# Kernel tuning notes

Hardware: AMD Instinct MI355X
Metric: run time of the kernel (lower is better)

The kernel has to match this reference:

```python
import jax, jax.numpy as jnp
import numpy as np

N = 100000   # nodes
E = 1600000  # edges (avg degree 16)
D = 128      # in_dim == out_dim (residual path)
NEG_SLOPE = 0.1


def setup_inputs() -> dict:
    key = jax.random.key(0)
    k1, k2, k3 = jax.random.split(key, 3)
    x = jax.random.normal(k1, (N, D), dtype=jnp.float32)
    edge_index = jax.random.randint(k2, (2, E), 0, N, dtype=jnp.int32)
    # GCNConv linear weight (stored as [in, out]; PyG uses x @ W^T with [out, in] — same math)
    W = jax.random.normal(k3, (D, D), dtype=jnp.float32) / np.sqrt(D).astype(np.float32)
    b = jnp.zeros((D,), dtype=jnp.float32)
    return {"x": x, "edge_index": edge_index, "W": W, "b": b}


def reference(x, edge_index, W, b):
    n = x.shape[0]
    # add self loops (GCNConv add_self_loops=True)
    loops = jnp.arange(n, dtype=edge_index.dtype)
    src = jnp.concatenate([edge_index[0], loops])
    dst = jnp.concatenate([edge_index[1], loops])
    # symmetric normalization: deg computed on destination index (PyG gcn_norm)
    deg = jax.ops.segment_sum(jnp.ones_like(dst, dtype=x.dtype), dst, num_segments=n)
    dinv = jnp.where(deg > 0, jax.lax.rsqrt(deg), 0.0)
    norm = dinv[src] * dinv[dst]                     # [E+N]
    # transform-then-propagate: small GEMM, then gather/scale/scatter
    h = x @ W                                        # [N, D]
    msgs = h[src] * norm[:, None]                    # [E+N, D] gather + scale
    agg = jax.ops.segment_sum(msgs, dst, num_segments=n) + b  # scatter-add
    act = jnp.where(agg >= 0, agg, NEG_SLOPE * agg)  # leaky_relu(0.1)
    return act + x                                   # residual (in_dim == out_dim)
```

## Files before the change

### kernel.cpp

```cpp
#include <hip/hip_runtime.h>
#include <hip/hip_bf16.h>

#define D 128
#define NEG_SLOPE 0.1f
#define BSHIFT 7
#define BSIZE 128
#define HALF 64
#define SRCBITS 17
#define SRCMASK 0x1FFFF
#define NBMAX 784
#define REGION 2432
#define SRCCAP 1536

typedef __attribute__((ext_vector_type(8))) short bf16x8;
typedef __attribute__((ext_vector_type(4))) float f32x4;
typedef __attribute__((ext_vector_type(2))) float f32x2;

__device__ inline unsigned short f2bf(float f) {
    unsigned u = __builtin_bit_cast(unsigned, f);
    u += 0x7fff + ((u >> 16) & 1);
    return (unsigned short)(u >> 16);
}

__global__ __launch_bounds__(512) void k_scatter2(const int* __restrict__ src, const int* __restrict__ dst,
                                                  int* __restrict__ cursor, int* __restrict__ ebuf,
                                                  int E, int NB,
                                                  const float* __restrict__ W,
                                                  unsigned short* __restrict__ Wt) {
    int b = blockIdx.x;
    int nbE = gridDim.x - 32;
    if (b >= nbE) {
        int tt = (b - nbE) * 512 + threadIdx.x;
        int k = tt >> 7, nn = tt & 127;
        Wt[nn * D + k] = f2bf(W[k * D + nn]);
        return;
    }
    __shared__ int cntL[NBMAX], baseL[NBMAX], curL[NBMAX];
    int t = threadIdx.x;
    for (int i = t; i < NB; i += 512) { cntL[i] = 0; curL[i] = 0; }
    __syncthreads();

    const int4* src4 = (const int4*)src;
    const int4* dst4 = (const int4*)dst;
    int sv[16], dv[16];
    int nval[4];
#pragma unroll
    for (int j = 0; j < 4; j++) {
        int i4 = b * 2048 + j * 512 + t;
        int e = i4 * 4;
        if (e + 4 <= E) {
            int4 s = src4[i4];
            int4 d = dst4[i4];
            sv[j * 4] = s.x; sv[j * 4 + 1] = s.y; sv[j * 4 + 2] = s.z; sv[j * 4 + 3] = s.w;
            dv[j * 4] = d.x; dv[j * 4 + 1] = d.y; dv[j * 4 + 2] = d.z; dv[j * 4 + 3] = d.w;
            nval[j] = 4;
        } else {
            int c = 0;
            for (int k = e; k < E; k++, c++) { sv[j * 4 + c] = src[k]; dv[j * 4 + c] = dst[k]; }
            nval[j] = c;
        }
    }
#pragma unroll
    for (int j = 0; j < 4; j++)
        for (int k = 0; k < nval[j]; k++) atomicAdd(&cntL[dv[j * 4 + k] >> BSHIFT], 1);
    __syncthreads();
    for (int i = t; i < NB; i += 512) {
        int c = cntL[i];
        if (c) baseL[i] = atomicAdd(&cursor[i], c);
    }
    __syncthreads();
#pragma unroll
    for (int j = 0; j < 4; j++)
        for (int k = 0; k < nval[j]; k++) {
            int d = dv[j * 4 + k];
            int bk = d >> BSHIFT;
            int slot = baseL[bk] + atomicAdd(&curL[bk], 1);
            if (slot < REGION)
                ebuf[bk * REGION + slot] = ((d & (BSIZE - 1)) << SRCBITS) | sv[j * 4 + k];
        }
}

__global__ __launch_bounds__(256) void k_gemm(const float* __restrict__ x,
                                              const unsigned short* __restrict__ Wt,
                                              const int* __restrict__ bucketCnt,
                                              const int* __restrict__ ebuf,
                                              unsigned char* __restrict__ h, int n) {
    __shared__ unsigned short Wl[D * 136];
    __shared__ int cntL[BSIZE];
    int t = threadIdx.x;
    if (t < BSIZE) cntL[t] = 0;
    const uint4* Wg4 = (const uint4*)Wt;
#pragma unroll
    for (int j = 0; j < 8; j++) {
        int c = t + 256 * j;
        int row = c >> 4, kg = c & 15;
        *(uint4*)&Wl[row * 136 + kg * 8] = Wg4[row * 16 + kg];
    }
    __syncthreads();

    int estart = blockIdx.x * REGION;
    int ecnt = bucketCnt[blockIdx.x];
    if (ecnt > REGION) ecnt = REGION;
    for (int e = t; e < ecnt; e += 256) atomicAdd(&cntL[ebuf[estart + e] >> SRCBITS], 1);

    int lane = t & 63, wave = t >> 6;
    int quad = lane >> 4, mrow = lane & 15;
    int rbase = blockIdx.x * 128 + wave * 32;

    const float4* x4 = (const float4*)x;
    float4 a0[2][4], a1[2][4];
#pragma unroll
    for (int rt = 0; rt < 2; rt++) {
        int row = rbase + rt * 16 + mrow;
        long rowl = (row < n) ? row : (n - 1);
#pragma unroll
        for (int ks = 0; ks < 4; ks++) {
            long base = rowl * 32 + ks * 8 + quad * 2;
            a0[rt][ks] = x4[base];
            a1[rt][ks] = x4[base + 1];
        }
    }
    bf16x8 af[2][4];
#pragma unroll
    for (int rt = 0; rt < 2; rt++)
#pragma unroll
        for (int ks = 0; ks < 4; ks++) {
            bf16x8 f;
            f[0] = (short)f2bf(a0[rt][ks].x); f[1] = (short)f2bf(a0[rt][ks].y);
            f[2] = (short)f2bf(a0[rt][ks].z); f[3] = (short)f2bf(a0[rt][ks].w);
            f[4] = (short)f2bf(a1[rt][ks].x); f[5] = (short)f2bf(a1[rt][ks].y);
            f[6] = (short)f2bf(a1[rt][ks].z); f[7] = (short)f2bf(a1[rt][ks].w);
            af[rt][ks] = f;
        }

    f32x4 acc[2][8];
#pragma unroll
    for (int rt = 0; rt < 2; rt++)
#pragma unroll
        for (int ct = 0; ct < 8; ct++) acc[rt][ct] = (f32x4){0.f, 0.f, 0.f, 0.f};

#pragma unroll
    for (int ks = 0; ks < 4; ks++) {
#pragma unroll
        for (int ct = 0; ct < 8; ct++) {
            bf16x8 bf = *(bf16x8*)&Wl[(ct * 16 + mrow) * 136 + ks * 32 + quad * 8];
#pragma unroll
            for (int rt = 0; rt < 2; rt++)
                acc[rt][ct] = __builtin_amdgcn_mfma_f32_16x16x32_bf16(af[rt][ks], bf, acc[rt][ct], 0, 0, 0);
        }
    }

    __syncthreads();

#pragma unroll
    for (int rt = 0; rt < 2; rt++) {
#pragma unroll
        for (int reg = 0; reg < 4; reg++) {
            int row = rbase + rt * 16 + quad * 4 + reg;
            if (row < n) {
                int rloc = wave * 32 + rt * 16 + quad * 4 + reg;
                float dv = rsqrtf((float)cntL[rloc] + 1.0f);
                float a[8];
#pragma unroll
                for (int ct = 0; ct < 8; ct++) a[ct] = acc[rt][ct][reg] * dv;
                int w0 = __builtin_amdgcn_cvt_pk_fp8_f32(a[0], a[1], 0, false);
                w0 = __builtin_amdgcn_cvt_pk_fp8_f32(a[2], a[3], w0, true);
                int w1 = __builtin_amdgcn_cvt_pk_fp8_f32(a[4], a[5], 0, false);
                w1 = __builtin_amdgcn_cvt_pk_fp8_f32(a[6], a[7], w1, true);
                uint2 wv; wv.x = (unsigned)w0; wv.y = (unsigned)w1;
                *(uint2*)&h[(long)row * 128 + mrow * 8] = wv;
            }
        }
    }
}

#define ACCV(v)                                                       \
    {                                                                 \
        acc2[0] += __builtin_amdgcn_cvt_pk_f32_fp8((int)(v).x, false);\
        acc2[1] += __builtin_amdgcn_cvt_pk_f32_fp8((int)(v).x, true); \
        acc2[2] += __builtin_amdgcn_cvt_pk_f32_fp8((int)(v).y, false);\
        acc2[3] += __builtin_amdgcn_cvt_pk_f32_fp8((int)(v).y, true); \
        acc2[4] += __builtin_amdgcn_cvt_pk_f32_fp8((int)(v).z, false);\
        acc2[5] += __builtin_amdgcn_cvt_pk_f32_fp8((int)(v).z, true); \
        acc2[6] += __builtin_amdgcn_cvt_pk_f32_fp8((int)(v).w, false);\
        acc2[7] += __builtin_amdgcn_cvt_pk_f32_fp8((int)(v).w, true); \
    }

__global__ __launch_bounds__(256) void k_aggregate(const uint4* __restrict__ h4, const float* __restrict__ x,
                                                   const float* __restrict__ bias,
                                                   const int* __restrict__ bucketCnt, const int* __restrict__ ebuf,
                                                   float* __restrict__ out, int N) {
    __shared__ int srcL[SRCCAP];
    __shared__ int degL[HALF];
    __shared__ int startL[HALF];
    __shared__ int curL[HALF];

    int b = blockIdx.x >> 1, half = blockIdx.x & 1;
    int t = threadIdx.x;
    int nstart = (b << BSHIFT) + half * HALF;
    int estart = b * REGION;
    int ecnt = bucketCnt[b];
    if (ecnt > REGION) ecnt = REGION;

    if (t < HALF) degL[t] = 0;
    __syncthreads();

    int ev[10];
    int ne = 0;
    for (int e = t; e < ecnt; e += 256) ev[ne++] = ebuf[estart + e];
    for (int k = 0; k < ne; k++) {
        int dl = ev[k] >> SRCBITS;
        if ((dl >> 6) == half) atomicAdd(&degL[dl & (HALF - 1)], 1);
    }
    __syncthreads();

    if (t < 64) {
        int d = degL[t];
        int inc = d;
        for (int sh = 1; sh < 64; sh <<= 1) {
            int y = __shfl_up(inc, sh, 64);
            if (t >= sh) inc += y;
        }
        startL[t] = inc - d;
        curL[t] = inc - d;
    }
    __syncthreads();
    for (int k = 0; k < ne; k++) {
        int dl = ev[k] >> SRCBITS;
        if ((dl >> 6) == half) {
            int pos = atomicAdd(&curL[dl & (HALF - 1)], 1);
            if (pos < SRCCAP) srcL[pos] = ev[k] & SRCMASK;
        }
    }
    __syncthreads();

    int wave = t >> 6, lane = t & 63;
    int slot = lane >> 3, chunk = lane & 7;
    for (int nloc = wave; nloc < HALF; nloc += 4) {
        int i = nstart + nloc;
        if (i >= N) break;
        int start = startL[nloc], m = degL[nloc];
        if (start + m > SRCCAP) m = (SRCCAP > start) ? SRCCAP - start : 0;

        f32x2 acc2[8];
#pragma unroll
        for (int r = 0; r < 8; r++) acc2[r] = (f32x2){0.f, 0.f};
        if (slot == 0) {
            uint4 v = h4[(long)i * 8 + chunk];
            ACCV(v);
        }

        int j0 = 0;
        if (m >= 16) {
            int ja = start + slot;
            int e0 = srcL[ja], e1 = srcL[ja + 8];
            for (;;) {
                uint4 v0 = h4[(long)e0 * 8 + chunk];
                uint4 v1 = h4[(long)e1 * 8 + chunk];
                j0 += 16;
                bool more = (j0 + 16 <= m);
                if (more) {
                    int jb = start + j0 + slot;
                    e0 = srcL[jb];
                    e1 = srcL[jb + 8];
                }
                ACCV(v0);
                ACCV(v1);
                if (!more) break;
            }
        }
        if (j0 + 8 <= m) {
            int e = srcL[start + j0 + slot];
            uint4 v = h4[(long)e * 8 + chunk];
            ACCV(v);
            j0 += 8;
        }
        for (int j = j0 + slot; j < m; j += 8) {
            int e = srcL[start + j];
            uint4 v = h4[(long)e * 8 + chunk];
            ACCV(v);
        }

#pragma unroll
        for (int r = 0; r < 8; r++) {
            acc2[r].x += __shfl_xor(acc2[r].x, 8, 64);
            acc2[r].x += __shfl_xor(acc2[r].x, 16, 64);
            acc2[r].x += __shfl_xor(acc2[r].x, 32, 64);
            acc2[r].y += __shfl_xor(acc2[r].y, 8, 64);
            acc2[r].y += __shfl_xor(acc2[r].y, 16, 64);
            acc2[r].y += __shfl_xor(acc2[r].y, 32, 64);
        }

        int s1 = slot >> 1;
        f32x2 eL = (s1 == 0) ? acc2[0] : (s1 == 1) ? acc2[1] : (s1 == 2) ? acc2[2] : acc2[3];
        f32x2 eH = (s1 == 0) ? acc2[4] : (s1 == 1) ? acc2[5] : (s1 == 2) ? acc2[6] : acc2[7];
        float ax = (slot & 1) ? eL.y : eL.x;
        float ay = (slot & 1) ? eH.y : eH.x;

        float di = rsqrtf((float)m + 1.0f);
        int dbase = slot * 16 + chunk * 2;
        float2 bb = *(const float2*)&bias[dbase];
        float2 xv = *(const float2*)&x[(long)i * D + dbase];
        ax = ax * di + bb.x;
        ay = ay * di + bb.y;
        ax = (ax >= 0.f) ? ax : NEG_SLOPE * ax;
        ay = (ay >= 0.f) ? ay : NEG_SLOPE * ay;
        float2 o;
        o.x = ax + xv.x;
        o.y = ay + xv.y;
        *(float2*)&out[(long)i * D + dbase] = o;
    }
}

extern "C" void kernel_launch(void* const* d_in, const int* in_sizes, int n_in,
                              void* d_out, int out_size, void* d_ws, size_t ws_size,
                              hipStream_t stream) {
    const float* x = (const float*)d_in[0];
    const int* edge_index = (const int*)d_in[1];
    const float* W = (const float*)d_in[2];
    const float* bias = (const float*)d_in[3];
    float* out = (float*)d_out;

    int N = in_sizes[0] / D;
    int E = in_sizes[1] / 2;
    const int* src = edge_index;
    const int* dst = edge_index + E;
    int NB = (N + BSIZE - 1) >> BSHIFT;

    char* ws = (char*)d_ws;
    size_t off = 0;
    auto alloc = [&](size_t bytes) {
        void* p = ws + off;
        off += (bytes + 15) & ~(size_t)15;
        return p;
    };
    int* cursor = (int*)alloc((size_t)NB * 4);
    int* ebuf = (int*)alloc((size_t)NB * REGION * 4);
    unsigned short* Wt = (unsigned short*)alloc((size_t)D * D * 2);
    unsigned char* h = (unsigned char*)alloc((size_t)N * D);

    int nbE = (E + 8191) / 8192;

    hipMemsetAsync(cursor, 0, (size_t)NB * 4, stream);
    k_scatter2<<<nbE + 32, 512, 0, stream>>>(src, dst, cursor, ebuf, E, NB, W, Wt);
    k_gemm<<<(N + 127) / 128, 256, 0, stream>>>(x, Wt, cursor, ebuf, h, N);
    k_aggregate<<<NB * 2, 256, 0, stream>>>((const uint4*)h, x, bias, cursor, ebuf, out, N);
}
```

Measured before the change: 209.6 us.

## Use one 512-thread aggregate block per bucket and halve scatter edges per block

The aggregate kernel now processes a whole 128-node bucket per 512-thread block instead of two 64-node halves in 256-thread blocks. This removes the duplicated read and filtering of each bucket's edge list and drops the SRCCAP truncation. The scatter kernel now handles 4096 edges per block with fixed unrolled loops and sentinel-padded tails instead of variable-length inner loops, which doubles its block count. The change trades fewer aggregate blocks and more shared memory per block for less redundant edge work.

```diff
diff --git a/kernel.cpp b/kernel.cpp
--- a/kernel.cpp
+++ b/kernel.cpp
@@ -5,12 +5,10 @@
 #define NEG_SLOPE 0.1f
 #define BSHIFT 7
 #define BSIZE 128
-#define HALF 64
 #define SRCBITS 17
 #define SRCMASK 0x1FFFF
 #define NBMAX 784
 #define REGION 2432
-#define SRCCAP 1536
 
 typedef __attribute__((ext_vector_type(8))) short bf16x8;
 typedef __attribute__((ext_vector_type(4))) float f32x4;
@@ -42,27 +40,27 @@
 
     const int4* src4 = (const int4*)src;
     const int4* dst4 = (const int4*)dst;
-    int sv[16], dv[16];
-    int nval[4];
-#pragma unroll
-    for (int j = 0; j < 4; j++) {
-        int i4 = b * 2048 + j * 512 + t;
+    int sv[8], dv[8];
+#pragma unroll
+    for (int j = 0; j < 2; j++) {
+        int i4 = b * 1024 + j * 512 + t;
         int e = i4 * 4;
+        int4 s, d;
         if (e + 4 <= E) {
-            int4 s = src4[i4];
-            int4 d = dst4[i4];
-            sv[j * 4] = s.x; sv[j * 4 + 1] = s.y; sv[j * 4 + 2] = s.z; sv[j * 4 + 3] = s.w;
-            dv[j * 4] = d.x; dv[j * 4 + 1] = d.y; dv[j * 4 + 2] = d.z; dv[j * 4 + 3] = d.w;
-            nval[j] = 4;
+            s = src4[i4];
+            d = dst4[i4];
         } else {
-            int c = 0;
-            for (int k = e; k < E; k++, c++) { sv[j * 4 + c] = src[k]; dv[j * 4 + c] = dst[k]; }
-            nval[j] = c;
-        }
-    }
-#pragma unroll
-    for (int j = 0; j < 4; j++)
-        for (int k = 0; k < nval[j]; k++) atomicAdd(&cntL[dv[j * 4 + k] >> BSHIFT], 1);
+            s.x = (e < E) ? src[e] : 0;     d.x = (e < E) ? dst[e] : -1;
+            s.y = (e + 1 < E) ? src[e + 1] : 0; d.y = (e + 1 < E) ? dst[e + 1] : -1;
+            s.z = (e + 2 < E) ? src[e + 2] : 0; d.z = (e + 2 < E) ? dst[e + 2] : -1;
+            s.w = (e + 3 < E) ? src[e + 3] : 0; d.w = (e + 3 < E) ? dst[e + 3] : -1;
+        }
+        sv[j * 4 + 0] = s.x; sv[j * 4 + 1] = s.y; sv[j * 4 + 2] = s.z; sv[j * 4 + 3] = s.w;
+        dv[j * 4 + 0] = d.x; dv[j * 4 + 1] = d.y; dv[j * 4 + 2] = d.z; dv[j * 4 + 3] = d.w;
+    }
+#pragma unroll
+    for (int k = 0; k < 8; k++)
+        if (dv[k] >= 0) atomicAdd(&cntL[dv[k] >> BSHIFT], 1);
     __syncthreads();
     for (int i = t; i < NB; i += 512) {
         int c = cntL[i];
@@ -70,14 +68,15 @@
     }
     __syncthreads();
 #pragma unroll
-    for (int j = 0; j < 4; j++)
-        for (int k = 0; k < nval[j]; k++) {
-            int d = dv[j * 4 + k];
+    for (int k = 0; k < 8; k++) {
+        int d = dv[k];
+        if (d >= 0) {
             int bk = d >> BSHIFT;
             int slot = baseL[bk] + atomicAdd(&curL[bk], 1);
             if (slot < REGION)
-                ebuf[bk * REGION + slot] = ((d & (BSIZE - 1)) << SRCBITS) | sv[j * 4 + k];
-        }
+                ebuf[bk * REGION + slot] = ((d & (BSIZE - 1)) << SRCBITS) | sv[k];
+        }
+    }
 }
 
 __global__ __launch_bounds__(256) void k_gemm(const float* __restrict__ x,
@@ -186,61 +185,66 @@
         acc2[7] += __builtin_amdgcn_cvt_pk_f32_fp8((int)(v).w, true); \
     }
 
-__global__ __launch_bounds__(256) void k_aggregate(const uint4* __restrict__ h4, const float* __restrict__ x,
+__global__ __launch_bounds__(512) void k_aggregate(const uint4* __restrict__ h4, const float* __restrict__ x,
                                                    const float* __restrict__ bias,
                                                    const int* __restrict__ bucketCnt, const int* __restrict__ ebuf,
                                                    float* __restrict__ out, int N) {
-    __shared__ int srcL[SRCCAP];
-    __shared__ int degL[HALF];
-    __shared__ int startL[HALF];
-    __shared__ int curL[HALF];
-
-    int b = blockIdx.x >> 1, half = blockIdx.x & 1;
+    __shared__ int srcL[REGION];
+    __shared__ int degL[BSIZE];
+    __shared__ int startL[BSIZE];
+    __shared__ int curL[BSIZE];
+
+    int b = blockIdx.x;
     int t = threadIdx.x;
-    int nstart = (b << BSHIFT) + half * HALF;
+    int nstart = b << BSHIFT;
     int estart = b * REGION;
     int ecnt = bucketCnt[b];
     if (ecnt > REGION) ecnt = REGION;
 
-    if (t < HALF) degL[t] = 0;
-    __syncthreads();
-
-    int ev[10];
-    int ne = 0;
-    for (int e = t; e < ecnt; e += 256) ev[ne++] = ebuf[estart + e];
-    for (int k = 0; k < ne; k++) {
-        int dl = ev[k] >> SRCBITS;
-        if ((dl >> 6) == half) atomicAdd(&degL[dl & (HALF - 1)], 1);
-    }
+    if (t < BSIZE) degL[t] = 0;
+    __syncthreads();
+
+    int ev[5];
+#pragma unroll
+    for (int k = 0; k < 5; k++) {
+        int e = t + k * 512;
+        ev[k] = (e < ecnt) ? ebuf[estart + e] : -1;
+    }
+#pragma unroll
+    for (int k = 0; k < 5; k++)
+        if (ev[k] >= 0) atomicAdd(&degL[ev[k] >> SRCBITS], 1);
     __syncthreads();
 
     if (t < 64) {
-        int d = degL[t];
-        int inc = d;
+        int d0 = degL[2 * t], d1 = degL[2 * t + 1];
+        int sum = d0 + d1;
+        int inc = sum;
         for (int sh = 1; sh < 64; sh <<= 1) {
             int y = __shfl_up(inc, sh, 64);
             if (t >= sh) inc += y;
         }
-        startL[t] = inc - d;
-        curL[t] = inc - d;
-    }
-    __syncthreads();
-    for (int k = 0; k < ne; k++) {
-        int dl = ev[k] >> SRCBITS;
-        if ((dl >> 6) == half) {
-            int pos = atomicAdd(&curL[dl & (HALF - 1)], 1);
-            if (pos < SRCCAP) srcL[pos] = ev[k] & SRCMASK;
-        }
-    }
+        int e0 = inc - sum;
+        startL[2 * t] = e0;
+        startL[2 * t + 1] = e0 + d0;
+        curL[2 * t] = e0;
+        curL[2 * t + 1] = e0 + d0;
+    }
+    __syncthreads();
+#pragma unroll
+    for (int k = 0; k < 5; k++)
+        if (ev[k] >= 0) {
+            int v = ev[k];
+            int pos = atomicAdd(&curL[v >> SRCBITS], 1);
+            srcL[pos] = v & SRCMASK;
+        }
     __syncthreads();
 
     int wave = t >> 6, lane = t & 63;
     int slot = lane >> 3, chunk = lane & 7;
-    for (int nloc = wave; nloc < HALF; nloc += 4) {
+    for (int nloc = wave; nloc < BSIZE; nloc += 8) {
         int i = nstart + nloc;
         if (i >= N) break;
         int start = startL[nloc], m = degL[nloc];
-        if (start + m > SRCCAP) m = (SRCCAP > start) ? SRCCAP - start : 0;
 
         f32x2 acc2[8];
 #pragma unroll
@@ -339,10 +343,10 @@
     unsigned short* Wt = (unsigned short*)alloc((size_t)D * D * 2);
     unsigned char* h = (unsigned char*)alloc((size_t)N * D);
 
-    int nbE = (E + 8191) / 8192;
+    int nbE = (E + 4095) / 4096;
 
     hipMemsetAsync(cursor, 0, (size_t)NB * 4, stream);
     k_scatter2<<<nbE + 32, 512, 0, stream>>>(src, dst, cursor, ebuf, E, NB, W, Wt);
-    k_gemm<<<(N + 127) / 128, 256, 0, stream>>>(x, Wt, cursor, ebuf, h, N);
-    k_aggregate<<<NB * 2, 256, 0, stream>>>((const uint4*)h, x, bias, cursor, ebuf, out, N);
-}
+    k_gemm<<<NB, 256, 0, stream>>>(x, Wt, cursor, ebuf, h, N);
+    k_aggregate<<<NB, 512, 0, stream>>>((const uint4*)h, x, bias, cursor, ebuf, out, N);
+}
```

Measured after the change: 217.7 us. +3.9%, slower.
